# Kernel optimization log

Measured on AMD Instinct MI355X. Metric: run time of the kernel, lower is better.

The kernel has to match this reference:

```python
import jax, jax.numpy as jnp
import numpy as np

N_NODES = 50000
N_EDGES = 1600000


def gcn_conv(h, W, b, src, dst, ew, n_nodes):
    """PyG GCNConv: linear -> add self-loops (weight 1) -> sym-norm scatter-add -> bias."""
    h = h @ W                                   # [N, out]
    loop = jnp.arange(n_nodes, dtype=src.dtype)
    s = jnp.concatenate([src, loop])            # [E+N]
    d = jnp.concatenate([dst, loop])
    w = jnp.concatenate([ew, jnp.ones((n_nodes,), dtype=h.dtype)])
    deg = jax.ops.segment_sum(w, d, num_segments=n_nodes)          # in-degree (weighted)
    dinv = jnp.where(deg > 0, jax.lax.rsqrt(deg), 0.0)
    coef = dinv[s] * w * dinv[d]                # D^-1/2 A D^-1/2 per-edge coefficient
    msg = h[s] * coef[:, None]                  # gather + scale  [E+N, out]
    out = jax.ops.segment_sum(msg, d, num_segments=n_nodes)        # scatter-add
    return out + b


def setup_inputs() -> dict:
    key = jax.random.key(0)
    ks = jax.random.split(key, 6)
    x = jax.random.normal(ks[0], (N_NODES, 256), dtype=jnp.float32)
    edge_index = jax.random.randint(ks[1], (2, N_EDGES), 0, N_NODES, dtype=jnp.int64)
    edge_weight = jax.random.uniform(ks[2], (N_EDGES,), dtype=jnp.float32)
    W1 = jax.random.normal(ks[3], (256, 128), dtype=jnp.float32) * (1.0 / np.sqrt(256))
    b1 = jnp.zeros((128,), dtype=jnp.float32)
    W2 = jax.random.normal(ks[4], (128, 64), dtype=jnp.float32) * (1.0 / np.sqrt(128))
    b2 = jnp.zeros((64,), dtype=jnp.float32)
    return {"x": x, "edge_index": edge_index, "edge_weight": edge_weight,
            "W1": W1, "b1": b1, "W2": W2, "b2": b2}


def reference(x, edge_index, edge_weight, W1, b1, W2, b2):
    src, dst = edge_index[0], edge_index[1]
    n = x.shape[0]
    h = gcn_conv(x, W1, b1, src, dst, edge_weight, n)
    h = jax.nn.relu(h)
    # dropout is identity in eval mode
    out = gcn_conv(h, W2, b2, src, dst, edge_weight, n)
    return out
```

## Files before the change

### kernel.cpp

```cpp
#include <hip/hip_runtime.h>

#define NN 50000
#define NE 1600000
#define NB 391
#define NBLK 512
#define EPB 3125
#define CAP 4992

typedef short bf16x8 __attribute__((ext_vector_type(8)));
typedef float f32x4 __attribute__((ext_vector_type(4)));

static __device__ __forceinline__ unsigned f2bf(float f) {
    union { float f; unsigned u; } v; v.f = f;
    return (v.u + 0x7FFF + ((v.u >> 16) & 1)) >> 16;
}

static __device__ __forceinline__ void acc8(float* acc, uint4 h, float c) {
    const unsigned* u = (const unsigned*)&h;
    #pragma unroll
    for (int q = 0; q < 4; ++q) {
        acc[2*q]   += __uint_as_float(u[q] << 16) * c;
        acc[2*q+1] += __uint_as_float(u[q] & 0xFFFF0000u) * c;
    }
}

__global__ __launch_bounds__(256) void k1_scatter(const int* __restrict__ src,
        const int* __restrict__ dst, const float* __restrict__ ew,
        int* __restrict__ cursor, int2* __restrict__ ebuf,
        const float* __restrict__ W1, const float* __restrict__ W2,
        ushort* __restrict__ Wt1, ushort* __restrict__ Wt2) {
    int blk = blockIdx.x;
    int t = threadIdx.x;
    if (blk >= NBLK) {
        for (int idx = (blk - NBLK) * 256 + t; idx < 40960; idx += 32 * 256) {
            if (idx < 32768) {
                int k = idx >> 7, n = idx & 127;
                Wt1[n * 256 + k] = (ushort)f2bf(W1[idx]);
            } else {
                int i = idx - 32768;
                int k = i >> 6, n = i & 63;
                Wt2[n * 128 + k] = (ushort)f2bf(W2[i]);
            }
        }
        return;
    }
    __shared__ int h[NB];
    __shared__ int curs[NB];
    __shared__ int sdst[EPB];
    for (int i = t; i < NB; i += 256) h[i] = 0;
    __syncthreads();
    int base = blk * EPB;
    for (int k = t; k < EPB; k += 256) {
        int d = dst[base + k];
        sdst[k] = d;
        atomicAdd(&h[d >> 7], 1);
    }
    __syncthreads();
    for (int i = t; i < NB; i += 256)
        curs[i] = i * CAP + atomicAdd(&cursor[i], h[i]);
    __syncthreads();
    for (int k = t; k < EPB; k += 256) {
        int d = sdst[k];
        int s = src[base + k];
        float w = ew[base + k];
        int pos = atomicAdd(&curs[d >> 7], 1);
        ebuf[pos] = make_int2(s | ((d & 127) << 16), __float_as_int(w));
    }
}

__global__ __launch_bounds__(512) void p4_build(const int2* __restrict__ ebuf,
        const int* __restrict__ cursor, unsigned* __restrict__ edata,
        float* __restrict__ dinv, int2* __restrict__ rowptr2) {
    __shared__ int cnt[128], loff[128], cur[128], sd[128];
    __shared__ float deg[128];
    __shared__ int2 se[CAP];
    int bk = blockIdx.x;
    int t = threadIdx.x;
    int ebase = bk * CAP;
    int ecnt = cursor[bk];
    if (ecnt > CAP) ecnt = CAP;
    if (t < 128) { cnt[t] = 0; cur[t] = 0; deg[t] = 0.0f; }
    __syncthreads();
    for (int i = t; i < ecnt; i += 512) {
        int2 e = ebuf[ebase + i];
        se[i] = e;
        int dl = (e.x >> 16) & 127;
        atomicAdd(&cnt[dl], 1);
        atomicAdd(&deg[dl], __int_as_float(e.y));
    }
    __syncthreads();
    if (t < 128) sd[t] = (cnt[t] + 3) & ~3;
    __syncthreads();
    for (int off = 1; off < 128; off <<= 1) {
        int v = 0;
        if (t < 128 && t >= off) v = sd[t - off];
        __syncthreads();
        if (t < 128) sd[t] += v;
        __syncthreads();
    }
    if (t < 128) {
        int cp = (cnt[t] + 3) & ~3;
        loff[t] = sd[t] - cp;
    }
    __syncthreads();
    int node = bk * 128 + t;
    if (t < 128 && node < NN) {
        dinv[node] = rsqrtf(deg[t] + 1.0f);
        int cp = (cnt[t] + 3) & ~3;
        int beg = ebase + loff[t];
        rowptr2[node] = make_int2(beg, beg + cp);
        for (int i = cnt[t]; i < cp; ++i)
            edata[ebase + loff[t] + i] = 0;
    }
    for (int i = t; i < ecnt; i += 512) {
        int2 e = se[i];
        int dl = (e.x >> 16) & 127;
        int slot = loff[dl] + atomicAdd(&cur[dl], 1);
        edata[ebase + slot] = (unsigned)(e.x & 0xFFFF)
                            | (f2bf(__int_as_float(e.y)) << 16);
    }
}

__global__ __launch_bounds__(256) void gemm1_kernel(const float* __restrict__ A,
        const ushort* __restrict__ Bt, ushort* __restrict__ C,
        const float* __restrict__ dinv, int M) {
    const int K = 256, N = 128;
    __shared__ __align__(16) ushort As[64][72];
    __shared__ __align__(16) ushort Bs[128][72];
    int tid = threadIdx.x;
    int bm = blockIdx.x * 64;
    int w = tid >> 6, lane = tid & 63;
    int m = lane & 15, quad = lane >> 4;
    f32x4 acc[8] = {};
    int ra = tid >> 2, ksa = (tid & 3) * 16;
    int rb = tid >> 1, ksb = (tid & 1) * 32;
    int grow = bm + ra; if (grow >= M) grow = M - 1;
    const float* ap = A + (size_t)grow * K + ksa;
    const ushort* bp = Bt + (size_t)rb * K + ksb;
    for (int k0 = 0; k0 < K; k0 += 64) {
        float4 f0 = *(const float4*)(ap + k0);
        float4 f1 = *(const float4*)(ap + k0 + 4);
        float4 f2 = *(const float4*)(ap + k0 + 8);
        float4 f3 = *(const float4*)(ap + k0 + 12);
        uint4 bv0 = *(const uint4*)(bp + k0);
        uint4 bv1 = *(const uint4*)(bp + k0 + 8);
        uint4 bv2 = *(const uint4*)(bp + k0 + 16);
        uint4 bv3 = *(const uint4*)(bp + k0 + 24);
        uint4 pa, pb;
        pa.x = f2bf(f0.x) | (f2bf(f0.y) << 16);
        pa.y = f2bf(f0.z) | (f2bf(f0.w) << 16);
        pa.z = f2bf(f1.x) | (f2bf(f1.y) << 16);
        pa.w = f2bf(f1.z) | (f2bf(f1.w) << 16);
        pb.x = f2bf(f2.x) | (f2bf(f2.y) << 16);
        pb.y = f2bf(f2.z) | (f2bf(f2.w) << 16);
        pb.z = f2bf(f3.x) | (f2bf(f3.y) << 16);
        pb.w = f2bf(f3.z) | (f2bf(f3.w) << 16);
        __syncthreads();
        *(uint4*)&As[ra][ksa] = pa;
        *(uint4*)&As[ra][ksa + 8] = pb;
        *(uint4*)&Bs[rb][ksb] = bv0;
        *(uint4*)&Bs[rb][ksb + 8] = bv1;
        *(uint4*)&Bs[rb][ksb + 16] = bv2;
        *(uint4*)&Bs[rb][ksb + 24] = bv3;
        __syncthreads();
        #pragma unroll
        for (int ks = 0; ks < 2; ++ks) {
            bf16x8 a = *(const bf16x8*)&As[w * 16 + m][ks * 32 + quad * 8];
            #pragma unroll
            for (int t = 0; t < 8; ++t) {
                bf16x8 b = *(const bf16x8*)&Bs[t * 16 + m][ks * 32 + quad * 8];
                acc[t] = __builtin_amdgcn_mfma_f32_16x16x32_bf16(a, b, acc[t], 0, 0, 0);
            }
        }
    }
    int rbase = bm + w * 16 + quad * 4;
    float dv[4];
    #pragma unroll
    for (int rg = 0; rg < 4; ++rg)
        dv[rg] = (rbase + rg < M) ? dinv[rbase + rg] : 0.0f;
    #pragma unroll
    for (int t = 0; t < 8; ++t) {
        int col = t * 16 + m;
        #pragma unroll
        for (int rg = 0; rg < 4; ++rg) {
            int row = rbase + rg;
            if (row < M)
                C[(size_t)row * N + col] = (ushort)f2bf(dv[rg] * acc[t][rg]);
        }
    }
}

__global__ __launch_bounds__(256) void agg1_fused_kernel(
        const int2* __restrict__ rowptr2, const unsigned* __restrict__ edata,
        const ushort* __restrict__ H, const float* __restrict__ dinv,
        const float* __restrict__ bias, const ushort* __restrict__ Wt2,
        ushort* __restrict__ H2) {
    __shared__ __align__(16) ushort Ats[16][136];
    int tid = threadIdx.x;
    int nl = tid >> 4;
    int node = blockIdx.x * 16 + nl;
    int glane = tid & 15;
    int2 rp = rowptr2[node];
    int beg = rp.x, end = rp.y;
    float acc[8] = {};
    const ushort* Hl = H + (size_t)glane * 8;
    int e = beg;
    int n8 = beg + ((end - beg) & ~7);
    for (; e < n8; e += 8) {
        unsigned m0 = edata[e];
        unsigned m1 = edata[e + 1];
        unsigned m2 = edata[e + 2];
        unsigned m3 = edata[e + 3];
        unsigned m4 = edata[e + 4];
        unsigned m5 = edata[e + 5];
        unsigned m6 = edata[e + 6];
        unsigned m7 = edata[e + 7];
        uint4 h0 = *(const uint4*)(Hl + (size_t)(m0 & 0xFFFF) * 128);
        uint4 h1 = *(const uint4*)(Hl + (size_t)(m1 & 0xFFFF) * 128);
        uint4 h2 = *(const uint4*)(Hl + (size_t)(m2 & 0xFFFF) * 128);
        uint4 h3 = *(const uint4*)(Hl + (size_t)(m3 & 0xFFFF) * 128);
        uint4 h4 = *(const uint4*)(Hl + (size_t)(m4 & 0xFFFF) * 128);
        uint4 h5 = *(const uint4*)(Hl + (size_t)(m5 & 0xFFFF) * 128);
        uint4 h6 = *(const uint4*)(Hl + (size_t)(m6 & 0xFFFF) * 128);
        uint4 h7 = *(const uint4*)(Hl + (size_t)(m7 & 0xFFFF) * 128);
        acc8(acc, h0, __uint_as_float(m0 & 0xFFFF0000u));
        acc8(acc, h1, __uint_as_float(m1 & 0xFFFF0000u));
        acc8(acc, h2, __uint_as_float(m2 & 0xFFFF0000u));
        acc8(acc, h3, __uint_as_float(m3 & 0xFFFF0000u));
        acc8(acc, h4, __uint_as_float(m4 & 0xFFFF0000u));
        acc8(acc, h5, __uint_as_float(m5 & 0xFFFF0000u));
        acc8(acc, h6, __uint_as_float(m6 & 0xFFFF0000u));
        acc8(acc, h7, __uint_as_float(m7 & 0xFFFF0000u));
    }
    if (e < end) {
        unsigned m0 = edata[e];
        unsigned m1 = edata[e + 1];
        unsigned m2 = edata[e + 2];
        unsigned m3 = edata[e + 3];
        uint4 h0 = *(const uint4*)(Hl + (size_t)(m0 & 0xFFFF) * 128);
        uint4 h1 = *(const uint4*)(Hl + (size_t)(m1 & 0xFFFF) * 128);
        uint4 h2 = *(const uint4*)(Hl + (size_t)(m2 & 0xFFFF) * 128);
        uint4 h3 = *(const uint4*)(Hl + (size_t)(m3 & 0xFFFF) * 128);
        acc8(acc, h0, __uint_as_float(m0 & 0xFFFF0000u));
        acc8(acc, h1, __uint_as_float(m1 & 0xFFFF0000u));
        acc8(acc, h2, __uint_as_float(m2 & 0xFFFF0000u));
        acc8(acc, h3, __uint_as_float(m3 & 0xFFFF0000u));
    }
    float di = dinv[node];
    uint4 hn = *(const uint4*)(Hl + (size_t)node * 128);
    const unsigned* un = (const unsigned*)&hn;
    float4 bv0 = *(const float4*)(bias + glane * 8);
    float4 bv1 = *(const float4*)(bias + glane * 8 + 4);
    float v[8];
    #pragma unroll
    for (int q = 0; q < 4; ++q) {
        v[2*q]   = di * (acc[2*q]   + __uint_as_float(un[q] << 16));
        v[2*q+1] = di * (acc[2*q+1] + __uint_as_float(un[q] & 0xFFFF0000u));
    }
    v[0] += bv0.x; v[1] += bv0.y; v[2] += bv0.z; v[3] += bv0.w;
    v[4] += bv1.x; v[5] += bv1.y; v[6] += bv1.z; v[7] += bv1.w;
    #pragma unroll
    for (int k = 0; k < 8; ++k) v[k] = fmaxf(v[k], 0.0f);
    uint4 o;
    o.x = f2bf(v[0]) | (f2bf(v[1]) << 16);
    o.y = f2bf(v[2]) | (f2bf(v[3]) << 16);
    o.z = f2bf(v[4]) | (f2bf(v[5]) << 16);
    o.w = f2bf(v[6]) | (f2bf(v[7]) << 16);
    *(uint4*)&Ats[nl][glane * 8] = o;
    __syncthreads();
    int w = tid >> 6, lane = tid & 63;
    int m = lane & 15, quad = lane >> 4;
    const ushort* bp = Wt2 + (size_t)(w * 16 + m) * 128 + quad * 8;
    f32x4 c2 = {};
    #pragma unroll
    for (int kc = 0; kc < 4; ++kc) {
        bf16x8 a = *(const bf16x8*)&Ats[m][kc * 32 + quad * 8];
        bf16x8 b = *(const bf16x8*)(bp + kc * 32);
        c2 = __builtin_amdgcn_mfma_f32_16x16x32_bf16(a, b, c2, 0, 0, 0);
    }
    int rbase = blockIdx.x * 16 + quad * 4;
    #pragma unroll
    for (int rg = 0; rg < 4; ++rg) {
        float dvr = dinv[rbase + rg];
        H2[(size_t)(rbase + rg) * 64 + w * 16 + m] = (ushort)f2bf(dvr * c2[rg]);
    }
}

__global__ __launch_bounds__(256) void agg2_kernel(
        const int2* __restrict__ rowptr2, const unsigned* __restrict__ edata,
        const ushort* __restrict__ H, const float* __restrict__ dinv,
        const float* __restrict__ bias, float* __restrict__ out) {
    int node = blockIdx.x * 32 + (threadIdx.x >> 3);
    if (node >= NN) return;
    int glane = threadIdx.x & 7;
    int2 rp = rowptr2[node];
    int beg = rp.x, end = rp.y;
    float acc[8] = {};
    const ushort* Hl = H + (size_t)glane * 8;
    int e = beg;
    int n8 = beg + ((end - beg) & ~7);
    for (; e < n8; e += 8) {
        unsigned m0 = edata[e];
        unsigned m1 = edata[e + 1];
        unsigned m2 = edata[e + 2];
        unsigned m3 = edata[e + 3];
        unsigned m4 = edata[e + 4];
        unsigned m5 = edata[e + 5];
        unsigned m6 = edata[e + 6];
        unsigned m7 = edata[e + 7];
        uint4 h0 = *(const uint4*)(Hl + (size_t)(m0 & 0xFFFF) * 64);
        uint4 h1 = *(const uint4*)(Hl + (size_t)(m1 & 0xFFFF) * 64);
        uint4 h2 = *(const uint4*)(Hl + (size_t)(m2 & 0xFFFF) * 64);
        uint4 h3 = *(const uint4*)(Hl + (size_t)(m3 & 0xFFFF) * 64);
        uint4 h4 = *(const uint4*)(Hl + (size_t)(m4 & 0xFFFF) * 64);
        uint4 h5 = *(const uint4*)(Hl + (size_t)(m5 & 0xFFFF) * 64);
        uint4 h6 = *(const uint4*)(Hl + (size_t)(m6 & 0xFFFF) * 64);
        uint4 h7 = *(const uint4*)(Hl + (size_t)(m7 & 0xFFFF) * 64);
        acc8(acc, h0, __uint_as_float(m0 & 0xFFFF0000u));
        acc8(acc, h1, __uint_as_float(m1 & 0xFFFF0000u));
        acc8(acc, h2, __uint_as_float(m2 & 0xFFFF0000u));
        acc8(acc, h3, __uint_as_float(m3 & 0xFFFF0000u));
        acc8(acc, h4, __uint_as_float(m4 & 0xFFFF0000u));
        acc8(acc, h5, __uint_as_float(m5 & 0xFFFF0000u));
        acc8(acc, h6, __uint_as_float(m6 & 0xFFFF0000u));
        acc8(acc, h7, __uint_as_float(m7 & 0xFFFF0000u));
    }
    if (e < end) {
        unsigned m0 = edata[e];
        unsigned m1 = edata[e + 1];
        unsigned m2 = edata[e + 2];
        unsigned m3 = edata[e + 3];
        uint4 h0 = *(const uint4*)(Hl + (size_t)(m0 & 0xFFFF) * 64);
        uint4 h1 = *(const uint4*)(Hl + (size_t)(m1 & 0xFFFF) * 64);
        uint4 h2 = *(const uint4*)(Hl + (size_t)(m2 & 0xFFFF) * 64);
        uint4 h3 = *(const uint4*)(Hl + (size_t)(m3 & 0xFFFF) * 64);
        acc8(acc, h0, __uint_as_float(m0 & 0xFFFF0000u));
        acc8(acc, h1, __uint_as_float(m1 & 0xFFFF0000u));
        acc8(acc, h2, __uint_as_float(m2 & 0xFFFF0000u));
        acc8(acc, h3, __uint_as_float(m3 & 0xFFFF0000u));
    }
    float di = dinv[node];
    uint4 hn = *(const uint4*)(Hl + (size_t)node * 64);
    const unsigned* un = (const unsigned*)&hn;
    float4 bv0 = *(const float4*)(bias + glane * 8);
    float4 bv1 = *(const float4*)(bias + glane * 8 + 4);
    float v[8];
    #pragma unroll
    for (int q = 0; q < 4; ++q) {
        v[2*q]   = di * (acc[2*q]   + __uint_as_float(un[q] << 16));
        v[2*q+1] = di * (acc[2*q+1] + __uint_as_float(un[q] & 0xFFFF0000u));
    }
    v[0] += bv0.x; v[1] += bv0.y; v[2] += bv0.z; v[3] += bv0.w;
    v[4] += bv1.x; v[5] += bv1.y; v[6] += bv1.z; v[7] += bv1.w;
    float* o = out + (size_t)node * 64 + glane * 8;
    *(float4*)(o)     = make_float4(v[0], v[1], v[2], v[3]);
    *(float4*)(o + 4) = make_float4(v[4], v[5], v[6], v[7]);
}

extern "C" void kernel_launch(void* const* d_in, const int* in_sizes, int n_in,
                              void* d_out, int out_size, void* d_ws, size_t ws_size,
                              hipStream_t stream) {
    const float* x  = (const float*)d_in[0];
    const int*   ei = (const int*)d_in[1];
    const float* ew = (const float*)d_in[2];
    const float* W1 = (const float*)d_in[3];
    const float* b1 = (const float*)d_in[4];
    const float* W2 = (const float*)d_in[5];
    const float* b2 = (const float*)d_in[6];
    const int* src = ei;
    const int* dst = ei + NE;
    float* out = (float*)d_out;

    float*  ws      = (float*)d_ws;
    float*  dinv    = ws;
    int2*   rowptr2 = (int2*)(ws + 50048);
    int*    cursor  = (int*)(ws + 150144);
    ushort* Wt1     = (ushort*)(ws + 150656);
    ushort* Wt2     = Wt1 + 32768;
    unsigned* edata = (unsigned*)(ws + 171136);
    ushort* H1      = (ushort*)(ws + 2123008);
    ushort* H2      = (ushort*)(ws + 5323008);
    int2*   ebuf    = (int2*)H1;

    hipMemsetAsync(cursor, 0, NB * sizeof(int), stream);
    k1_scatter<<<NBLK + 32, 256, 0, stream>>>(src, dst, ew, cursor, ebuf,
                                              W1, W2, Wt1, Wt2);
    p4_build<<<NB, 512, 0, stream>>>(ebuf, cursor, edata, dinv, rowptr2);

    gemm1_kernel<<<782, 256, 0, stream>>>(x, Wt1, H1, dinv, NN);
    agg1_fused_kernel<<<3125, 256, 0, stream>>>(rowptr2, edata, H1, dinv, b1, Wt2, H2);
    agg2_kernel<<<1563, 256, 0, stream>>>(rowptr2, edata, H2, dinv, b2, out);
}
```

Measured before the change: 245.2 us.

## Quantize layer-1 features to int8 with per-row scales folded into edge weights

Layer-1 hidden features are stored as per-row symmetric int8, offset by 128, instead of bf16. A new pass folds each source row's scale into the bf16 edge coefficient, and the aggregation subtracts the offset through a running coefficient sum. The feature layout is permuted so the packed bytes line up with a permuted W2 and bias. This halves the gather traffic in the heaviest aggregation, at the cost of an extra edge-rewrite kernel, more int-to-float conversion work, and lower precision that may breach the accuracy tolerance. Edge metadata loads are also vectorized to uint4 in both aggregation kernels.

```diff
diff --git a/kernel.cpp b/kernel.cpp
--- a/kernel.cpp
+++ b/kernel.cpp
@@ -24,22 +24,40 @@
     }
 }
 
+static __device__ __forceinline__ void accq(float* acc, float& cs, uint2 g, float c) {
+    cs += c;
+    acc[0] += (float)(g.x & 0xffu) * c;
+    acc[1] += (float)((g.x >> 8) & 0xffu) * c;
+    acc[2] += (float)((g.x >> 16) & 0xffu) * c;
+    acc[3] += (float)(g.x >> 24) * c;
+    acc[4] += (float)(g.y & 0xffu) * c;
+    acc[5] += (float)((g.y >> 8) & 0xffu) * c;
+    acc[6] += (float)((g.y >> 16) & 0xffu) * c;
+    acc[7] += (float)(g.y >> 24) * c;
+}
+
 __global__ __launch_bounds__(256) void k1_scatter(const int* __restrict__ src,
         const int* __restrict__ dst, const float* __restrict__ ew,
         int* __restrict__ cursor, int2* __restrict__ ebuf,
         const float* __restrict__ W1, const float* __restrict__ W2,
-        ushort* __restrict__ Wt1, ushort* __restrict__ Wt2) {
+        const float* __restrict__ b1,
+        ushort* __restrict__ Wt1, ushort* __restrict__ Wt2,
+        float* __restrict__ b1p) {
     int blk = blockIdx.x;
     int t = threadIdx.x;
     if (blk >= NBLK) {
-        for (int idx = (blk - NBLK) * 256 + t; idx < 40960; idx += 32 * 256) {
+        for (int idx = (blk - NBLK) * 256 + t; idx < 41088; idx += 32 * 256) {
             if (idx < 32768) {
                 int k = idx >> 7, n = idx & 127;
                 Wt1[n * 256 + k] = (ushort)f2bf(W1[idx]);
-            } else {
+            } else if (idx < 40960) {
                 int i = idx - 32768;
                 int k = i >> 6, n = i & 63;
-                Wt2[n * 128 + k] = (ushort)f2bf(W2[i]);
+                int kp = ((k & 15) << 3) | (k >> 4);
+                Wt2[n * 128 + kp] = (ushort)f2bf(W2[i]);
+            } else {
+                int k = idx - 40960;
+                b1p[((k & 15) << 3) | (k >> 4)] = b1[k];
             }
         }
         return;
@@ -122,9 +140,9 @@
 }
 
 __global__ __launch_bounds__(256) void gemm1_kernel(const float* __restrict__ A,
-        const ushort* __restrict__ Bt, ushort* __restrict__ C,
-        const float* __restrict__ dinv, int M) {
-    const int K = 256, N = 128;
+        const ushort* __restrict__ Bt, unsigned char* __restrict__ H1q,
+        float* __restrict__ sscale, const float* __restrict__ dinv, int M) {
+    const int K = 256;
     __shared__ __align__(16) ushort As[64][72];
     __shared__ __align__(16) ushort Bs[128][72];
     int tid = threadIdx.x;
@@ -179,22 +197,50 @@
     for (int rg = 0; rg < 4; ++rg)
         dv[rg] = (rbase + rg < M) ? dinv[rbase + rg] : 0.0f;
     #pragma unroll
-    for (int t = 0; t < 8; ++t) {
-        int col = t * 16 + m;
+    for (int rg = 0; rg < 4; ++rg) {
+        float val[8];
+        float mx = 0.0f;
         #pragma unroll
-        for (int rg = 0; rg < 4; ++rg) {
-            int row = rbase + rg;
-            if (row < M)
-                C[(size_t)row * N + col] = (ushort)f2bf(dv[rg] * acc[t][rg]);
+        for (int t = 0; t < 8; ++t) {
+            val[t] = dv[rg] * acc[t][rg];
+            mx = fmaxf(mx, fabsf(val[t]));
         }
-    }
+        #pragma unroll
+        for (int off = 1; off < 16; off <<= 1)
+            mx = fmaxf(mx, __shfl_xor(mx, off));
+        float s = mx * (1.0f / 127.0f);
+        float inv = (mx > 0.0f) ? 127.0f / mx : 0.0f;
+        unsigned d0 = 0, d1 = 0;
+        #pragma unroll
+        for (int t = 0; t < 4; ++t) {
+            unsigned q0 = (unsigned)(__float2int_rn(val[t] * inv) + 128);
+            unsigned q1 = (unsigned)(__float2int_rn(val[t + 4] * inv) + 128);
+            d0 |= (q0 & 255u) << (8 * t);
+            d1 |= (q1 & 255u) << (8 * t);
+        }
+        int row = rbase + rg;
+        if (row < M) {
+            *(uint2*)&H1q[(size_t)row * 128 + m * 8] = make_uint2(d0, d1);
+            if (m == 0) sscale[row] = s;
+        }
+    }
+}
+
+__global__ __launch_bounds__(256) void fix_edata(const unsigned* __restrict__ edata,
+        const float* __restrict__ sscale, unsigned* __restrict__ edata1, int total) {
+    int i = blockIdx.x * 256 + threadIdx.x;
+    if (i >= total) return;
+    unsigned e = edata[i];
+    float w = __uint_as_float(e & 0xFFFF0000u);
+    float c = w * sscale[e & 0xFFFF];
+    edata1[i] = (e & 0xFFFFu) | (f2bf(c) << 16);
 }
 
 __global__ __launch_bounds__(256) void agg1_fused_kernel(
-        const int2* __restrict__ rowptr2, const unsigned* __restrict__ edata,
-        const ushort* __restrict__ H, const float* __restrict__ dinv,
-        const float* __restrict__ bias, const ushort* __restrict__ Wt2,
-        ushort* __restrict__ H2) {
+        const int2* __restrict__ rowptr2, const unsigned* __restrict__ edata1,
+        const unsigned char* __restrict__ Hq, const float* __restrict__ sscale,
+        const float* __restrict__ dinv, const float* __restrict__ b1p,
+        const ushort* __restrict__ Wt2, ushort* __restrict__ H2) {
     __shared__ __align__(16) ushort Ats[16][136];
     int tid = threadIdx.x;
     int nl = tid >> 4;
@@ -203,60 +249,53 @@
     int2 rp = rowptr2[node];
     int beg = rp.x, end = rp.y;
     float acc[8] = {};
-    const ushort* Hl = H + (size_t)glane * 8;
+    float cs = 0.0f;
+    const unsigned char* Hql = Hq + glane * 8;
     int e = beg;
     int n8 = beg + ((end - beg) & ~7);
     for (; e < n8; e += 8) {
-        unsigned m0 = edata[e];
-        unsigned m1 = edata[e + 1];
-        unsigned m2 = edata[e + 2];
-        unsigned m3 = edata[e + 3];
-        unsigned m4 = edata[e + 4];
-        unsigned m5 = edata[e + 5];
-        unsigned m6 = edata[e + 6];
-        unsigned m7 = edata[e + 7];
-        uint4 h0 = *(const uint4*)(Hl + (size_t)(m0 & 0xFFFF) * 128);
-        uint4 h1 = *(const uint4*)(Hl + (size_t)(m1 & 0xFFFF) * 128);
-        uint4 h2 = *(const uint4*)(Hl + (size_t)(m2 & 0xFFFF) * 128);
-        uint4 h3 = *(const uint4*)(Hl + (size_t)(m3 & 0xFFFF) * 128);
-        uint4 h4 = *(const uint4*)(Hl + (size_t)(m4 & 0xFFFF) * 128);
-        uint4 h5 = *(const uint4*)(Hl + (size_t)(m5 & 0xFFFF) * 128);
-        uint4 h6 = *(const uint4*)(Hl + (size_t)(m6 & 0xFFFF) * 128);
-        uint4 h7 = *(const uint4*)(Hl + (size_t)(m7 & 0xFFFF) * 128);
-        acc8(acc, h0, __uint_as_float(m0 & 0xFFFF0000u));
-        acc8(acc, h1, __uint_as_float(m1 & 0xFFFF0000u));
-        acc8(acc, h2, __uint_as_float(m2 & 0xFFFF0000u));
-        acc8(acc, h3, __uint_as_float(m3 & 0xFFFF0000u));
-        acc8(acc, h4, __uint_as_float(m4 & 0xFFFF0000u));
-        acc8(acc, h5, __uint_as_float(m5 & 0xFFFF0000u));
-        acc8(acc, h6, __uint_as_float(m6 & 0xFFFF0000u));
-        acc8(acc, h7, __uint_as_float(m7 & 0xFFFF0000u));
+        uint4 ma = *(const uint4*)&edata1[e];
+        uint4 mb = *(const uint4*)&edata1[e + 4];
+        uint2 g0 = *(const uint2*)(Hql + (size_t)(ma.x & 0xFFFF) * 128);
+        uint2 g1 = *(const uint2*)(Hql + (size_t)(ma.y & 0xFFFF) * 128);
+        uint2 g2 = *(const uint2*)(Hql + (size_t)(ma.z & 0xFFFF) * 128);
+        uint2 g3 = *(const uint2*)(Hql + (size_t)(ma.w & 0xFFFF) * 128);
+        uint2 g4 = *(const uint2*)(Hql + (size_t)(mb.x & 0xFFFF) * 128);
+        uint2 g5 = *(const uint2*)(Hql + (size_t)(mb.y & 0xFFFF) * 128);
+        uint2 g6 = *(const uint2*)(Hql + (size_t)(mb.z & 0xFFFF) * 128);
+        uint2 g7 = *(const uint2*)(Hql + (size_t)(mb.w & 0xFFFF) * 128);
+        accq(acc, cs, g0, __uint_as_float(ma.x & 0xFFFF0000u));
+        accq(acc, cs, g1, __uint_as_float(ma.y & 0xFFFF0000u));
+        accq(acc, cs, g2, __uint_as_float(ma.z & 0xFFFF0000u));
+        accq(acc, cs, g3, __uint_as_float(ma.w & 0xFFFF0000u));
+        accq(acc, cs, g4, __uint_as_float(mb.x & 0xFFFF0000u));
+        accq(acc, cs, g5, __uint_as_float(mb.y & 0xFFFF0000u));
+        accq(acc, cs, g6, __uint_as_float(mb.z & 0xFFFF0000u));
+        accq(acc, cs, g7, __uint_as_float(mb.w & 0xFFFF0000u));
     }
     if (e < end) {
-        unsigned m0 = edata[e];
-        unsigned m1 = edata[e + 1];
-        unsigned m2 = edata[e + 2];
-        unsigned m3 = edata[e + 3];
-        uint4 h0 = *(const uint4*)(Hl + (size_t)(m0 & 0xFFFF) * 128);
-        uint4 h1 = *(const uint4*)(Hl + (size_t)(m1 & 0xFFFF) * 128);
-        uint4 h2 = *(const uint4*)(Hl + (size_t)(m2 & 0xFFFF) * 128);
-        uint4 h3 = *(const uint4*)(Hl + (size_t)(m3 & 0xFFFF) * 128);
-        acc8(acc, h0, __uint_as_float(m0 & 0xFFFF0000u));
-        acc8(acc, h1, __uint_as_float(m1 & 0xFFFF0000u));
-        acc8(acc, h2, __uint_as_float(m2 & 0xFFFF0000u));
-        acc8(acc, h3, __uint_as_float(m3 & 0xFFFF0000u));
+        uint4 ma = *(const uint4*)&edata1[e];
+        uint2 g0 = *(const uint2*)(Hql + (size_t)(ma.x & 0xFFFF) * 128);
+        uint2 g1 = *(const uint2*)(Hql + (size_t)(ma.y & 0xFFFF) * 128);
+        uint2 g2 = *(const uint2*)(Hql + (size_t)(ma.z & 0xFFFF) * 128);
+        uint2 g3 = *(const uint2*)(Hql + (size_t)(ma.w & 0xFFFF) * 128);
+        accq(acc, cs, g0, __uint_as_float(ma.x & 0xFFFF0000u));
+        accq(acc, cs, g1, __uint_as_float(ma.y & 0xFFFF0000u));
+        accq(acc, cs, g2, __uint_as_float(ma.z & 0xFFFF0000u));
+        accq(acc, cs, g3, __uint_as_float(ma.w & 0xFFFF0000u));
+    }
+    {
+        float ss = sscale[node];
+        uint2 gs = *(const uint2*)(Hql + (size_t)node * 128);
+        accq(acc, cs, gs, ss);
     }
     float di = dinv[node];
-    uint4 hn = *(const uint4*)(Hl + (size_t)node * 128);
-    const unsigned* un = (const unsigned*)&hn;
-    float4 bv0 = *(const float4*)(bias + glane * 8);
-    float4 bv1 = *(const float4*)(bias + glane * 8 + 4);
+    float corr = -128.0f * cs;
+    float4 bv0 = *(const float4*)(b1p + glane * 8);
+    float4 bv1 = *(const float4*)(b1p + glane * 8 + 4);
     float v[8];
     #pragma unroll
-    for (int q = 0; q < 4; ++q) {
-        v[2*q]   = di * (acc[2*q]   + __uint_as_float(un[q] << 16));
-        v[2*q+1] = di * (acc[2*q+1] + __uint_as_float(un[q] & 0xFFFF0000u));
-    }
+    for (int j = 0; j < 8; ++j) v[j] = di * (acc[j] + corr);
     v[0] += bv0.x; v[1] += bv0.y; v[2] += bv0.z; v[3] += bv0.w;
     v[4] += bv1.x; v[5] += bv1.y; v[6] += bv1.z; v[7] += bv1.w;
     #pragma unroll
@@ -300,44 +339,35 @@
     int e = beg;
     int n8 = beg + ((end - beg) & ~7);
     for (; e < n8; e += 8) {
-        unsigned m0 = edata[e];
-        unsigned m1 = edata[e + 1];
-        unsigned m2 = edata[e + 2];
-        unsigned m3 = edata[e + 3];
-        unsigned m4 = edata[e + 4];
-        unsigned m5 = edata[e + 5];
-        unsigned m6 = edata[e + 6];
-        unsigned m7 = edata[e + 7];
-        uint4 h0 = *(const uint4*)(Hl + (size_t)(m0 & 0xFFFF) * 64);
-        uint4 h1 = *(const uint4*)(Hl + (size_t)(m1 & 0xFFFF) * 64);
-        uint4 h2 = *(const uint4*)(Hl + (size_t)(m2 & 0xFFFF) * 64);
-        uint4 h3 = *(const uint4*)(Hl + (size_t)(m3 & 0xFFFF) * 64);
-        uint4 h4 = *(const uint4*)(Hl + (size_t)(m4 & 0xFFFF) * 64);
-        uint4 h5 = *(const uint4*)(Hl + (size_t)(m5 & 0xFFFF) * 64);
-        uint4 h6 = *(const uint4*)(Hl + (size_t)(m6 & 0xFFFF) * 64);
-        uint4 h7 = *(const uint4*)(Hl + (size_t)(m7 & 0xFFFF) * 64);
-        acc8(acc, h0, __uint_as_float(m0 & 0xFFFF0000u));
-        acc8(acc, h1, __uint_as_float(m1 & 0xFFFF0000u));
-        acc8(acc, h2, __uint_as_float(m2 & 0xFFFF0000u));
-        acc8(acc, h3, __uint_as_float(m3 & 0xFFFF0000u));
-        acc8(acc, h4, __uint_as_float(m4 & 0xFFFF0000u));
-        acc8(acc, h5, __uint_as_float(m5 & 0xFFFF0000u));
-        acc8(acc, h6, __uint_as_float(m6 & 0xFFFF0000u));
-        acc8(acc, h7, __uint_as_float(m7 & 0xFFFF0000u));
+        uint4 ma = *(const uint4*)&edata[e];
+        uint4 mb = *(const uint4*)&edata[e + 4];
+        uint4 h0 = *(const uint4*)(Hl + (size_t)(ma.x & 0xFFFF) * 64);
+        uint4 h1 = *(const uint4*)(Hl + (size_t)(ma.y & 0xFFFF) * 64);
+        uint4 h2 = *(const uint4*)(Hl + (size_t)(ma.z & 0xFFFF) * 64);
+        uint4 h3 = *(const uint4*)(Hl + (size_t)(ma.w & 0xFFFF) * 64);
+        uint4 h4 = *(const uint4*)(Hl + (size_t)(mb.x & 0xFFFF) * 64);
+        uint4 h5 = *(const uint4*)(Hl + (size_t)(mb.y & 0xFFFF) * 64);
+        uint4 h6 = *(const uint4*)(Hl + (size_t)(mb.z & 0xFFFF) * 64);
+        uint4 h7 = *(const uint4*)(Hl + (size_t)(mb.w & 0xFFFF) * 64);
+        acc8(acc, h0, __uint_as_float(ma.x & 0xFFFF0000u));
+        acc8(acc, h1, __uint_as_float(ma.y & 0xFFFF0000u));
+        acc8(acc, h2, __uint_as_float(ma.z & 0xFFFF0000u));
+        acc8(acc, h3, __uint_as_float(ma.w & 0xFFFF0000u));
+        acc8(acc, h4, __uint_as_float(mb.x & 0xFFFF0000u));
+        acc8(acc, h5, __uint_as_float(mb.y & 0xFFFF0000u));
+        acc8(acc, h6, __uint_as_float(mb.z & 0xFFFF0000u));
+        acc8(acc, h7, __uint_as_float(mb.w & 0xFFFF0000u));
     }
     if (e < end) {
-        unsigned m0 = edata[e];
-        unsigned m1 = edata[e + 1];
-        unsigned m2 = edata[e + 2];
-        unsigned m3 = edata[e + 3];
-        uint4 h0 = *(const uint4*)(Hl + (size_t)(m0 & 0xFFFF) * 64);
-        uint4 h1 = *(const uint4*)(Hl + (size_t)(m1 & 0xFFFF) * 64);
-        uint4 h2 = *(const uint4*)(Hl + (size_t)(m2 & 0xFFFF) * 64);
-        uint4 h3 = *(const uint4*)(Hl + (size_t)(m3 & 0xFFFF) * 64);
-        acc8(acc, h0, __uint_as_float(m0 & 0xFFFF0000u));
-        acc8(acc, h1, __uint_as_float(m1 & 0xFFFF0000u));
-        acc8(acc, h2, __uint_as_float(m2 & 0xFFFF0000u));
-        acc8(acc, h3, __uint_as_float(m3 & 0xFFFF0000u));
+        uint4 ma = *(const uint4*)&edata[e];
+        uint4 h0 = *(const uint4*)(Hl + (size_t)(ma.x & 0xFFFF) * 64);
+        uint4 h1 = *(const uint4*)(Hl + (size_t)(ma.y & 0xFFFF) * 64);
+        uint4 h2 = *(const uint4*)(Hl + (size_t)(ma.z & 0xFFFF) * 64);
+        uint4 h3 = *(const uint4*)(Hl + (size_t)(ma.w & 0xFFFF) * 64);
+        acc8(acc, h0, __uint_as_float(ma.x & 0xFFFF0000u));
+        acc8(acc, h1, __uint_as_float(ma.y & 0xFFFF0000u));
+        acc8(acc, h2, __uint_as_float(ma.z & 0xFFFF0000u));
+        acc8(acc, h3, __uint_as_float(ma.w & 0xFFFF0000u));
     }
     float di = dinv[node];
     uint4 hn = *(const uint4*)(Hl + (size_t)node * 64);
@@ -376,18 +406,24 @@
     int2*   rowptr2 = (int2*)(ws + 50048);
     int*    cursor  = (int*)(ws + 150144);
     ushort* Wt1     = (ushort*)(ws + 150656);
-    ushort* Wt2     = Wt1 + 32768;
-    unsigned* edata = (unsigned*)(ws + 171136);
-    ushort* H1      = (ushort*)(ws + 2123008);
-    ushort* H2      = (ushort*)(ws + 5323008);
-    int2*   ebuf    = (int2*)H1;
+    ushort* Wt2     = (ushort*)(ws + 167040);
+    float*  b1p     = ws + 171136;
+    float*  sscale  = ws + 171264;
+    unsigned* edata = (unsigned*)(ws + 221312);
+    unsigned* edata1= (unsigned*)(ws + 2173184);
+    unsigned char* H1q = (unsigned char*)(ws + 4125056);
+    ushort* H2      = (ushort*)(ws + 5725056);
+    int2*   ebuf    = (int2*)edata1;
 
     hipMemsetAsync(cursor, 0, NB * sizeof(int), stream);
     k1_scatter<<<NBLK + 32, 256, 0, stream>>>(src, dst, ew, cursor, ebuf,
-                                              W1, W2, Wt1, Wt2);
+                                              W1, W2, b1, Wt1, Wt2, b1p);
     p4_build<<<NB, 512, 0, stream>>>(ebuf, cursor, edata, dinv, rowptr2);
 
-    gemm1_kernel<<<782, 256, 0, stream>>>(x, Wt1, H1, dinv, NN);
-    agg1_fused_kernel<<<3125, 256, 0, stream>>>(rowptr2, edata, H1, dinv, b1, Wt2, H2);
+    gemm1_kernel<<<782, 256, 0, stream>>>(x, Wt1, H1q, sscale, dinv, NN);
+    fix_edata<<<(NB * CAP + 255) / 256, 256, 0, stream>>>(edata, sscale, edata1,
+                                                          NB * CAP);
+    agg1_fused_kernel<<<3125, 256, 0, stream>>>(rowptr2, edata1, H1q, sscale,
+                                                dinv, b1p, Wt2, H2);
     agg2_kernel<<<1563, 256, 0, stream>>>(rowptr2, edata, H2, dinv, b2, out);
 }
```

Result: faster. 227.8 us (-7.1%).
